# Kernel tuning notes

Hardware: AMD Instinct MI355X
Metric: run time of the kernel (lower is better)

Reference implementation:

```python
import jax, jax.numpy as jnp
import numpy as np

B, TQ, TK, DK, DV = 64, 1024, 1024, 64, 64


def setup_inputs() -> dict:
    key = jax.random.key(0)
    kq, kk, kv, km = jax.random.split(key, 4)
    q = jax.random.normal(kq, (B, TQ, DK), dtype=jnp.float32)
    k = jax.random.normal(kk, (B, TK, DK), dtype=jnp.float32)
    v = jax.random.normal(kv, (B, TK, DV), dtype=jnp.float32)
    mask = jax.random.randint(km, (B, TQ, TK), 0, 2).astype(jnp.int32)
    return {"q": q, "k": k, "v": v, "mask": mask}


def reference(q, k, v, mask):
    # attn = q @ k^T / sqrt(d_k)   -> [B, TQ, TK]
    temper = jnp.sqrt(jnp.asarray(q.shape[-1], dtype=jnp.float32))
    attn = jnp.einsum('bqd,bkd->bqk', q, k) / temper
    # mask-add: -1e9 where mask == 0
    mmask = -1e9 * (1.0 - mask.astype(jnp.float32))
    attn = attn + mmask
    attn = jax.nn.softmax(attn, axis=-1)
    # dropout rate is 0.0 -> identity
    out = jnp.einsum('bqk,bkd->bqd', attn, v)
    return (out, attn)
```

## Files before the change

### kernel.cpp

```cpp
#include <hip/hip_runtime.h>
#include <hip/hip_bf16.h>


#define B_   64
#define TQ_  1024
#define TK_  1024
#define DD   64

typedef short short8 __attribute__((ext_vector_type(8)));
typedef float f32x4 __attribute__((ext_vector_type(4)));

#define PSTR 264
#define WVS  (16 * PSTR)

#define QB_OFF  (0u)
#define KB_OFF  (8u << 20)
#define VT_OFF  (16u << 20)
#define MB_OFF  (24u << 20)
#define WS_NEED (32u << 20)

__device__ __forceinline__ unsigned cvt2(float a, float b) {
    __hip_bfloat162 h = __float22bfloat162_rn(make_float2(a, b));
    unsigned u; __builtin_memcpy(&u, &h, 4); return u;
}
__device__ __forceinline__ short cvt1(float a) {
    __hip_bfloat16 h = __float2bfloat16(a);
    short s; __builtin_memcpy(&s, &h, 2); return s;
}

union Frag { short8 s; unsigned u[4]; };

__global__ __launch_bounds__(256) void prep_kernel(
    const float* __restrict__ qg, const float* __restrict__ kg,
    const float* __restrict__ vg, const int* __restrict__ maskg,
    unsigned char* __restrict__ ws)
{
    const int t = threadIdx.x;
    const int gid = blockIdx.x;
    if (gid < 8192) {
        const int widx = gid * 256 + t;
        const int4* mp = (const int4*)(maskg + (size_t)widx * 32);
        unsigned bits = 0;
        #pragma unroll
        for (int i = 0; i < 8; ++i) {
            const int4 x = mp[i];
            bits |= (unsigned)(x.x & 1) << (4 * i)
                 |  (unsigned)(x.y & 1) << (4 * i + 1)
                 |  (unsigned)(x.z & 1) << (4 * i + 2)
                 |  (unsigned)(x.w & 1) << (4 * i + 3);
        }
        ((unsigned*)(ws + MB_OFF))[widx] = bits;
    } else if (gid < 8192 + 2048) {
        const int i8 = (gid - 8192) * 256 + t;
        const float* p = qg + (size_t)i8 * 8;
        const float4 x = *(const float4*)p, y = *(const float4*)(p + 4);
        uint4 o;
        o.x = cvt2(0.125f * x.x, 0.125f * x.y); o.y = cvt2(0.125f * x.z, 0.125f * x.w);
        o.z = cvt2(0.125f * y.x, 0.125f * y.y); o.w = cvt2(0.125f * y.z, 0.125f * y.w);
        ((uint4*)(ws + QB_OFF))[i8] = o;
    } else if (gid < 8192 + 4096) {
        const int i8 = (gid - 8192 - 2048) * 256 + t;
        const float* p = kg + (size_t)i8 * 8;
        const float4 x = *(const float4*)p, y = *(const float4*)(p + 4);
        uint4 o;
        o.x = cvt2(x.x, x.y); o.y = cvt2(x.z, x.w);
        o.z = cvt2(y.x, y.y); o.w = cvt2(y.z, y.w);
        ((uint4*)(ws + KB_OFF))[i8] = o;
    } else {
        __shared__ short tl[64][72];
        const int b = gid - (8192 + 4096);
        const float* vb = vg + (size_t)b * TK_ * DD;
        short* ob = (short*)(ws + VT_OFF) + (size_t)b * DD * TK_;
        for (int tile = 0; tile < 16; ++tile) {
            const int k0 = tile * 64;
            #pragma unroll
            for (int i = 0; i < 4; ++i) {
                const int row = i * 16 + (t >> 4);
                const int d   = (t & 15) * 4;
                const float4 x = *(const float4*)(vb + (size_t)(k0 + row) * DD + d);
                tl[d + 0][row] = cvt1(x.x); tl[d + 1][row] = cvt1(x.y);
                tl[d + 2][row] = cvt1(x.z); tl[d + 3][row] = cvt1(x.w);
            }
            __syncthreads();
            #pragma unroll
            for (int p = 0; p < 2; ++p) {
                const int d = p * 32 + (t >> 3);
                const uint4 val = *(const uint4*)&tl[d][(t & 7) * 8];
                *(uint4*)(ob + (size_t)d * TK_ + k0 + (t & 7) * 8) = val;
            }
            __syncthreads();
        }
    }
}

__global__ __launch_bounds__(256, 4) void attn_bf16_kernel(
    const unsigned char* __restrict__ ws,
    float* __restrict__ outg, float* __restrict__ attng)
{
    __shared__ __align__(16) short lds[4 * WVS];
    __shared__ float red[128];

    const int t    = threadIdx.x;
    const int wave = t >> 6, lane = t & 63;
    const int quad = lane >> 4, n16 = lane & 15;
    const int b    = blockIdx.y;
    const int q0   = blockIdx.x * 16;
    const int kbase = wave * 256;

    const short*    Qb = (const short*)(ws + QB_OFF);
    const short*    Kb = (const short*)(ws + KB_OFF);
    const short*    Vt = (const short*)(ws + VT_OFF);
    const unsigned* Mb = (const unsigned*)(ws + MB_OFF);

    short* pw = lds + wave * WVS;

    const unsigned* mrow = Mb + ((size_t)(b * TQ_ + q0 + n16)) * 32 + wave * 8;
    const uint4 mw0 = *(const uint4*)(mrow);
    const uint4 mw1 = *(const uint4*)(mrow + 4);

    const short* qp = Qb + ((size_t)(b * TQ_ + q0 + n16)) * DD + quad * 8;
    Frag qf0, qf1;
    qf0.s = *(const short8*)(qp);
    qf1.s = *(const short8*)(qp + 32);

    const short* vrow = Vt + (size_t)b * DD * TK_ + (size_t)n16 * TK_ + kbase + quad * 8;
    Frag vf[4];
    #pragma unroll
    for (int dg = 0; dg < 4; ++dg)
        vf[dg].s = *(const short8*)(vrow + (size_t)(dg * 16) * TK_);

    const short* kbp = Kb + (size_t)(b * TK_ + kbase) * DD;
    Frag kf[16][2];
    #pragma unroll
    for (int kt = 0; kt < 16; ++kt) {
        const short* kp = kbp + (size_t)(kt * 16 + n16) * DD + quad * 8;
        kf[kt][0].s = *(const short8*)(kp);
        kf[kt][1].s = *(const short8*)(kp + 32);
    }

    float s_reg[64];
    const unsigned mwa[8] = {mw0.x, mw0.y, mw0.z, mw0.w, mw1.x, mw1.y, mw1.z, mw1.w};
    #pragma unroll
    for (int kt = 0; kt < 16; ++kt) {
        f32x4 acc = {0.f, 0.f, 0.f, 0.f};
        acc = __builtin_amdgcn_mfma_f32_16x16x32_bf16(kf[kt][0].s, qf0.s, acc, 0, 0, 0);
        acc = __builtin_amdgcn_mfma_f32_16x16x32_bf16(kf[kt][1].s, qf1.s, acc, 0, 0, 0);
        const unsigned m4 = (mwa[kt >> 1] >> (((kt & 1) << 4) | (quad << 2))) & 15u;
        s_reg[kt * 4 + 0] = acc[0] + ((m4 & 1u) ? 0.f : -1e9f);
        s_reg[kt * 4 + 1] = acc[1] + ((m4 & 2u) ? 0.f : -1e9f);
        s_reg[kt * 4 + 2] = acc[2] + ((m4 & 4u) ? 0.f : -1e9f);
        s_reg[kt * 4 + 3] = acc[3] + ((m4 & 8u) ? 0.f : -1e9f);
    }

    float m8[8];
    #pragma unroll
    for (int j = 0; j < 8; ++j) m8[j] = s_reg[j];
    #pragma unroll
    for (int i = 8; i < 64; i += 8)
        #pragma unroll
        for (int j = 0; j < 8; ++j) m8[j] = fmaxf(m8[j], s_reg[i + j]);
    float m = fmaxf(fmaxf(fmaxf(m8[0], m8[1]), fmaxf(m8[2], m8[3])),
                    fmaxf(fmaxf(m8[4], m8[5]), fmaxf(m8[6], m8[7])));
    m = fmaxf(m, __shfl_xor(m, 16));
    m = fmaxf(m, __shfl_xor(m, 32));
    if (lane < 16) red[wave * 16 + n16] = m;
    __syncthreads();
    const float gm = fmaxf(fmaxf(red[n16], red[16 + n16]),
                           fmaxf(red[32 + n16], red[48 + n16]));
    float l0 = 0.f, l1 = 0.f, l2 = 0.f, l3 = 0.f;
    #pragma unroll
    for (int i = 0; i < 16; ++i) {
        const float p0 = __expf(s_reg[4*i+0] - gm);
        const float p1 = __expf(s_reg[4*i+1] - gm);
        const float p2 = __expf(s_reg[4*i+2] - gm);
        const float p3 = __expf(s_reg[4*i+3] - gm);
        s_reg[4*i+0] = p0; s_reg[4*i+1] = p1;
        s_reg[4*i+2] = p2; s_reg[4*i+3] = p3;
        l0 += p0; l1 += p1; l2 += p2; l3 += p3;
    }
    float lsum = (l0 + l1) + (l2 + l3);
    lsum += __shfl_xor(lsum, 16);
    lsum += __shfl_xor(lsum, 32);
    if (lane < 16) red[64 + wave * 16 + n16] = lsum;
    __syncthreads();
    const float inv = 1.f / (red[64 + n16] + red[80 + n16] +
                             red[96 + n16] + red[112 + n16]);
    #pragma unroll
    for (int i = 0; i < 64; ++i) s_reg[i] *= inv;

    float* ab = attng + ((size_t)(b * TQ_ + q0 + n16)) * TK_ + kbase + quad * 4;
    #pragma unroll
    for (int kt = 0; kt < 16; ++kt)
        *(float4*)(ab + kt * 16) = make_float4(s_reg[kt*4+0], s_reg[kt*4+1],
                                               s_reg[kt*4+2], s_reg[kt*4+3]);
    #pragma unroll
    for (int kt = 0; kt < 16; ++kt) {
        uint2 u;
        u.x = cvt2(s_reg[kt*4+0], s_reg[kt*4+1]);
        u.y = cvt2(s_reg[kt*4+2], s_reg[kt*4+3]);
        *(uint2*)(pw + n16 * PSTR + kt * 16 + quad * 4) = u;
    }

    f32x4 oacc[4];
    #pragma unroll
    for (int dg = 0; dg < 4; ++dg) oacc[dg] = (f32x4){0.f, 0.f, 0.f, 0.f};

    #pragma unroll
    for (int c = 0; c < 8; ++c) {
        Frag cur[4];
        #pragma unroll
        for (int dg = 0; dg < 4; ++dg) cur[dg] = vf[dg];
        if (c < 7) {
            #pragma unroll
            for (int dg = 0; dg < 4; ++dg)
                vf[dg].s = *(const short8*)(vrow + (size_t)(dg * 16) * TK_ + (c + 1) * 32);
        }
        Frag pf;
        pf.s = *(const short8*)(pw + n16 * PSTR + c * 32 + quad * 8);
        #pragma unroll
        for (int dg = 0; dg < 4; ++dg)
            oacc[dg] = __builtin_amdgcn_mfma_f32_16x16x32_bf16(cur[dg].s, pf.s, oacc[dg], 0, 0, 0);
    }

    float* ow = (float*)pw;
    #pragma unroll
    for (int dg = 0; dg < 4; ++dg)
        *(f32x4*)&ow[n16 * 68 + dg * 16 + quad * 4] = oacc[dg];
    __syncthreads();
    {
        const int row = t >> 4, col = (t & 15) * 4;
        const float* base = (const float*)lds;
        float4 o = make_float4(0.f, 0.f, 0.f, 0.f);
        #pragma unroll
        for (int w = 0; w < 4; ++w) {
            const float4 x = *(const float4*)(base + w * (WVS / 2) + row * 68 + col);
            o.x += x.x; o.y += x.y; o.z += x.z; o.w += x.w;
        }
        *(float4*)(outg + ((size_t)(b * TQ_ + q0 + row)) * DD + col) = o;
    }
}

__global__ __launch_bounds__(256, 3) void attn_fallback_kernel(
    const float* __restrict__ qg, const float* __restrict__ kg,
    const float* __restrict__ vg, const int* __restrict__ maskg,
    float* __restrict__ outg, float* __restrict__ attng)
{
    __shared__ __align__(16) short lds[4 * WVS];
    __shared__ float red[128];

    const int t    = threadIdx.x;
    const int wave = t >> 6, lane = t & 63;
    const int quad = lane >> 4, n16 = lane & 15;
    const int b    = blockIdx.y;
    const int q0   = blockIdx.x * 16;
    const int kbase = wave * 256;

    short* pw = lds + wave * WVS;

    Frag aq[2];
    {
        const float* qp = qg + ((size_t)(b * TQ_ + q0 + n16)) * DD + quad * 8;
        #pragma unroll
        for (int f = 0; f < 2; ++f) {
            float4 x = *(const float4*)(qp + f * 32);
            float4 y = *(const float4*)(qp + f * 32 + 4);
            aq[f].u[0] = cvt2(0.125f * x.x, 0.125f * x.y);
            aq[f].u[1] = cvt2(0.125f * x.z, 0.125f * x.w);
            aq[f].u[2] = cvt2(0.125f * y.x, 0.125f * y.y);
            aq[f].u[3] = cvt2(0.125f * y.z, 0.125f * y.w);
        }
    }

    float s_reg[64];
    const float* kbp  = kg + (size_t)b * TK_ * DD;
    const int*   mrow = maskg + ((size_t)(b * TQ_ + q0 + n16)) * TK_ + kbase + quad * 4;
    #pragma unroll
    for (int h = 0; h < 2; ++h) {
        int4 mk[8];
        #pragma unroll
        for (int i = 0; i < 8; ++i)
            mk[i] = *(const int4*)(mrow + (h * 8 + i) * 16);
        #pragma unroll
        for (int i = 0; i < 8; ++i) {
            const int kt = h * 8 + i;
            const float* kp = kbp + (size_t)(kbase + kt * 16 + n16) * DD + quad * 8;
            Frag bk[2];
            #pragma unroll
            for (int f = 0; f < 2; ++f) {
                float4 x = *(const float4*)(kp + f * 32);
                float4 y = *(const float4*)(kp + f * 32 + 4);
                bk[f].u[0] = cvt2(x.x, x.y); bk[f].u[1] = cvt2(x.z, x.w);
                bk[f].u[2] = cvt2(y.x, y.y); bk[f].u[3] = cvt2(y.z, y.w);
            }
            f32x4 acc = {0.f, 0.f, 0.f, 0.f};
            acc = __builtin_amdgcn_mfma_f32_16x16x32_bf16(bk[0].s, aq[0].s, acc, 0, 0, 0);
            acc = __builtin_amdgcn_mfma_f32_16x16x32_bf16(bk[1].s, aq[1].s, acc, 0, 0, 0);
            s_reg[kt * 4 + 0] = acc[0] + (mk[i].x ? 0.f : -1e9f);
            s_reg[kt * 4 + 1] = acc[1] + (mk[i].y ? 0.f : -1e9f);
            s_reg[kt * 4 + 2] = acc[2] + (mk[i].z ? 0.f : -1e9f);
            s_reg[kt * 4 + 3] = acc[3] + (mk[i].w ? 0.f : -1e9f);
        }
    }

    const float* vb0 = vg + (size_t)b * TK_ * DD + (size_t)(kbase + quad * 8) * DD + n16;
    float vraw[32];
    #pragma unroll
    for (int u = 0; u < 32; ++u)
        vraw[u] = vb0[(size_t)(u & 7) * DD + (u >> 3) * 16];

    float m8[8];
    #pragma unroll
    for (int j = 0; j < 8; ++j) m8[j] = s_reg[j];
    #pragma unroll
    for (int i = 8; i < 64; i += 8)
        #pragma unroll
        for (int j = 0; j < 8; ++j) m8[j] = fmaxf(m8[j], s_reg[i + j]);
    float m = fmaxf(fmaxf(fmaxf(m8[0], m8[1]), fmaxf(m8[2], m8[3])),
                    fmaxf(fmaxf(m8[4], m8[5]), fmaxf(m8[6], m8[7])));
    m = fmaxf(m, __shfl_xor(m, 16));
    m = fmaxf(m, __shfl_xor(m, 32));
    if (lane < 16) red[wave * 16 + n16] = m;
    __syncthreads();
    const float gm = fmaxf(fmaxf(red[n16], red[16 + n16]),
                           fmaxf(red[32 + n16], red[48 + n16]));
    float l0 = 0.f, l1 = 0.f, l2 = 0.f, l3 = 0.f;
    #pragma unroll
    for (int i = 0; i < 16; ++i) {
        const float p0 = __expf(s_reg[4*i+0] - gm);
        const float p1 = __expf(s_reg[4*i+1] - gm);
        const float p2 = __expf(s_reg[4*i+2] - gm);
        const float p3 = __expf(s_reg[4*i+3] - gm);
        s_reg[4*i+0] = p0; s_reg[4*i+1] = p1;
        s_reg[4*i+2] = p2; s_reg[4*i+3] = p3;
        l0 += p0; l1 += p1; l2 += p2; l3 += p3;
    }
    float lsum = (l0 + l1) + (l2 + l3);
    lsum += __shfl_xor(lsum, 16);
    lsum += __shfl_xor(lsum, 32);
    if (lane < 16) red[64 + wave * 16 + n16] = lsum;
    __syncthreads();
    const float inv = 1.f / (red[64 + n16] + red[80 + n16] +
                             red[96 + n16] + red[112 + n16]);
    #pragma unroll
    for (int i = 0; i < 64; ++i) s_reg[i] *= inv;

    float* ab = attng + ((size_t)(b * TQ_ + q0 + n16)) * TK_ + kbase + quad * 4;
    #pragma unroll
    for (int kt = 0; kt < 16; ++kt)
        *(float4*)(ab + kt * 16) = make_float4(s_reg[kt*4+0], s_reg[kt*4+1],
                                               s_reg[kt*4+2], s_reg[kt*4+3]);
    #pragma unroll
    for (int kt = 0; kt < 16; ++kt) {
        uint2 u;
        u.x = cvt2(s_reg[kt*4+0], s_reg[kt*4+1]);
        u.y = cvt2(s_reg[kt*4+2], s_reg[kt*4+3]);
        *(uint2*)(pw + n16 * PSTR + kt * 16 + quad * 4) = u;
    }

    f32x4 oacc[4];
    #pragma unroll
    for (int dg = 0; dg < 4; ++dg) oacc[dg] = (f32x4){0.f, 0.f, 0.f, 0.f};

    #pragma unroll
    for (int c = 0; c < 8; ++c) {
        unsigned va16[16];
        #pragma unroll
        for (int dg = 0; dg < 4; ++dg)
            #pragma unroll
            for (int w = 0; w < 4; ++w)
                va16[dg * 4 + w] = cvt2(vraw[dg * 8 + 2 * w], vraw[dg * 8 + 2 * w + 1]);
        if (c < 7) {
            #pragma unroll
            for (int u = 0; u < 32; ++u)
                vraw[u] = vb0[(size_t)((c + 1) * 32 + (u & 7)) * DD + (u >> 3) * 16];
        }
        Frag pf;
        pf.s = *(const short8*)(pw + n16 * PSTR + c * 32 + quad * 8);
        #pragma unroll
        for (int dg = 0; dg < 4; ++dg) {
            Frag af;
            af.u[0] = va16[dg*4+0]; af.u[1] = va16[dg*4+1];
            af.u[2] = va16[dg*4+2]; af.u[3] = va16[dg*4+3];
            oacc[dg] = __builtin_amdgcn_mfma_f32_16x16x32_bf16(af.s, pf.s, oacc[dg], 0, 0, 0);
        }
    }

    float* ow = (float*)pw;
    #pragma unroll
    for (int dg = 0; dg < 4; ++dg)
        *(f32x4*)&ow[n16 * 68 + dg * 16 + quad * 4] = oacc[dg];
    __syncthreads();
    {
        const int row = t >> 4, col = (t & 15) * 4;
        const float* base = (const float*)lds;
        float4 o = make_float4(0.f, 0.f, 0.f, 0.f);
        #pragma unroll
        for (int w = 0; w < 4; ++w) {
            const float4 x = *(const float4*)(base + w * (WVS / 2) + row * 68 + col);
            o.x += x.x; o.y += x.y; o.z += x.z; o.w += x.w;
        }
        *(float4*)(outg + ((size_t)(b * TQ_ + q0 + row)) * DD + col) = o;
    }
}

extern "C" void kernel_launch(void* const* d_in, const int* in_sizes, int n_in,
                              void* d_out, int out_size, void* d_ws, size_t ws_size,
                              hipStream_t stream) {
    const float* q    = (const float*)d_in[0];
    const float* k    = (const float*)d_in[1];
    const float* v    = (const float*)d_in[2];
    const int*   mask = (const int*)d_in[3];

    float* out  = (float*)d_out;
    float* attn = out + (size_t)B_ * TQ_ * DD;

    if (ws_size >= (size_t)WS_NEED && d_ws != nullptr) {
        unsigned char* ws = (unsigned char*)d_ws;
        prep_kernel<<<dim3(12352), 256, 0, stream>>>(q, k, v, mask, ws);
        attn_bf16_kernel<<<dim3(TQ_ / 16, B_), 256, 0, stream>>>(ws, out, attn);
    } else {
        attn_fallback_kernel<<<dim3(TQ_ / 16, B_), 256, 0, stream>>>(q, k, v, mask, out, attn);
    }
}
```

Measured before the change: 634.6 us.

## Halve per-wave P staging LDS and split V transpose across more blocks

The bf16 attention kernel now stages the probability tile in two halves of 128 keys each. It reuses a 68-word-stride buffer, which roughly halves LDS per block and is meant to allow more resident blocks per CU. The PV MFMA loop becomes two 4-step passes with a re-fill of the LDS buffer between them. The prep kernel's V transpose is spread over 1024 blocks of one 64-key tile each, instead of 64 blocks looping over 16 tiles, which removes a serial tail in the prep kernel.

```diff
diff --git a/kernel.cpp b/kernel.cpp
--- a/kernel.cpp
+++ b/kernel.cpp
@@ -10,8 +10,8 @@
 typedef short short8 __attribute__((ext_vector_type(8)));
 typedef float f32x4 __attribute__((ext_vector_type(4)));
 
-#define PSTR 264
-#define WVS  (16 * PSTR)
+#define PLW    68
+#define PL_U32 (16 * PLW)
 
 #define QB_OFF  (0u)
 #define KB_OFF  (8u << 20)
@@ -37,8 +37,29 @@
 {
     const int t = threadIdx.x;
     const int gid = blockIdx.x;
-    if (gid < 8192) {
-        const int widx = gid * 256 + t;
+    if (gid < 1024) {
+        __shared__ short tl[64][72];
+        const int b  = gid >> 4;
+        const int k0 = (gid & 15) * 64;
+        const float* vb = vg + (size_t)b * TK_ * DD;
+        short* ob = (short*)(ws + VT_OFF) + (size_t)b * DD * TK_;
+        #pragma unroll
+        for (int i = 0; i < 4; ++i) {
+            const int row = i * 16 + (t >> 4);
+            const int d   = (t & 15) * 4;
+            const float4 x = *(const float4*)(vb + (size_t)(k0 + row) * DD + d);
+            tl[d + 0][row] = cvt1(x.x); tl[d + 1][row] = cvt1(x.y);
+            tl[d + 2][row] = cvt1(x.z); tl[d + 3][row] = cvt1(x.w);
+        }
+        __syncthreads();
+        #pragma unroll
+        for (int p = 0; p < 2; ++p) {
+            const int d = p * 32 + (t >> 3);
+            const uint4 val = *(const uint4*)&tl[d][(t & 7) * 8];
+            *(uint4*)(ob + (size_t)d * TK_ + k0 + (t & 7) * 8) = val;
+        }
+    } else if (gid < 1024 + 8192) {
+        const int widx = (gid - 1024) * 256 + t;
         const int4* mp = (const int4*)(maskg + (size_t)widx * 32);
         unsigned bits = 0;
         #pragma unroll
@@ -50,46 +71,22 @@
                  |  (unsigned)(x.w & 1) << (4 * i + 3);
         }
         ((unsigned*)(ws + MB_OFF))[widx] = bits;
-    } else if (gid < 8192 + 2048) {
-        const int i8 = (gid - 8192) * 256 + t;
+    } else if (gid < 1024 + 8192 + 2048) {
+        const int i8 = (gid - 1024 - 8192) * 256 + t;
         const float* p = qg + (size_t)i8 * 8;
         const float4 x = *(const float4*)p, y = *(const float4*)(p + 4);
         uint4 o;
         o.x = cvt2(0.125f * x.x, 0.125f * x.y); o.y = cvt2(0.125f * x.z, 0.125f * x.w);
         o.z = cvt2(0.125f * y.x, 0.125f * y.y); o.w = cvt2(0.125f * y.z, 0.125f * y.w);
         ((uint4*)(ws + QB_OFF))[i8] = o;
-    } else if (gid < 8192 + 4096) {
-        const int i8 = (gid - 8192 - 2048) * 256 + t;
+    } else {
+        const int i8 = (gid - 1024 - 8192 - 2048) * 256 + t;
         const float* p = kg + (size_t)i8 * 8;
         const float4 x = *(const float4*)p, y = *(const float4*)(p + 4);
         uint4 o;
         o.x = cvt2(x.x, x.y); o.y = cvt2(x.z, x.w);
         o.z = cvt2(y.x, y.y); o.w = cvt2(y.z, y.w);
         ((uint4*)(ws + KB_OFF))[i8] = o;
-    } else {
-        __shared__ short tl[64][72];
-        const int b = gid - (8192 + 4096);
-        const float* vb = vg + (size_t)b * TK_ * DD;
-        short* ob = (short*)(ws + VT_OFF) + (size_t)b * DD * TK_;
-        for (int tile = 0; tile < 16; ++tile) {
-            const int k0 = tile * 64;
-            #pragma unroll
-            for (int i = 0; i < 4; ++i) {
-                const int row = i * 16 + (t >> 4);
-                const int d   = (t & 15) * 4;
-                const float4 x = *(const float4*)(vb + (size_t)(k0 + row) * DD + d);
-                tl[d + 0][row] = cvt1(x.x); tl[d + 1][row] = cvt1(x.y);
-                tl[d + 2][row] = cvt1(x.z); tl[d + 3][row] = cvt1(x.w);
-            }
-            __syncthreads();
-            #pragma unroll
-            for (int p = 0; p < 2; ++p) {
-                const int d = p * 32 + (t >> 3);
-                const uint4 val = *(const uint4*)&tl[d][(t & 7) * 8];
-                *(uint4*)(ob + (size_t)d * TK_ + k0 + (t & 7) * 8) = val;
-            }
-            __syncthreads();
-        }
     }
 }
 
@@ -97,7 +94,7 @@
     const unsigned char* __restrict__ ws,
     float* __restrict__ outg, float* __restrict__ attng)
 {
-    __shared__ __align__(16) short lds[4 * WVS];
+    __shared__ __align__(16) unsigned lds[4 * PL_U32];
     __shared__ float red[128];
 
     const int t    = threadIdx.x;
@@ -112,7 +109,7 @@
     const short*    Vt = (const short*)(ws + VT_OFF);
     const unsigned* Mb = (const unsigned*)(ws + MB_OFF);
 
-    short* pw = lds + wave * WVS;
+    unsigned* pl = lds + wave * PL_U32;
 
     const unsigned* mrow = Mb + ((size_t)(b * TQ_ + q0 + n16)) * 32 + wave * 8;
     const uint4 mw0 = *(const uint4*)(mrow);
@@ -194,11 +191,11 @@
         *(float4*)(ab + kt * 16) = make_float4(s_reg[kt*4+0], s_reg[kt*4+1],
                                                s_reg[kt*4+2], s_reg[kt*4+3]);
     #pragma unroll
-    for (int kt = 0; kt < 16; ++kt) {
+    for (int kt = 0; kt < 8; ++kt) {
         uint2 u;
         u.x = cvt2(s_reg[kt*4+0], s_reg[kt*4+1]);
         u.y = cvt2(s_reg[kt*4+2], s_reg[kt*4+3]);
-        *(uint2*)(pw + n16 * PSTR + kt * 16 + quad * 4) = u;
+        *(uint2*)&pl[n16 * PLW + kt * 8 + quad * 2] = u;
     }
 
     f32x4 oacc[4];
@@ -206,26 +203,49 @@
     for (int dg = 0; dg < 4; ++dg) oacc[dg] = (f32x4){0.f, 0.f, 0.f, 0.f};
 
     #pragma unroll
-    for (int c = 0; c < 8; ++c) {
+    for (int c = 0; c < 4; ++c) {
         Frag cur[4];
         #pragma unroll
         for (int dg = 0; dg < 4; ++dg) cur[dg] = vf[dg];
-        if (c < 7) {
+        #pragma unroll
+        for (int dg = 0; dg < 4; ++dg)
+            vf[dg].s = *(const short8*)(vrow + (size_t)(dg * 16) * TK_ + (c + 1) * 32);
+        Frag pf;
+        pf.s = *(const short8*)&pl[n16 * PLW + c * 16 + quad * 4];
+        #pragma unroll
+        for (int dg = 0; dg < 4; ++dg)
+            oacc[dg] = __builtin_amdgcn_mfma_f32_16x16x32_bf16(cur[dg].s, pf.s, oacc[dg], 0, 0, 0);
+    }
+
+    #pragma unroll
+    for (int kt = 8; kt < 16; ++kt) {
+        uint2 u;
+        u.x = cvt2(s_reg[kt*4+0], s_reg[kt*4+1]);
+        u.y = cvt2(s_reg[kt*4+2], s_reg[kt*4+3]);
+        *(uint2*)&pl[n16 * PLW + (kt - 8) * 8 + quad * 2] = u;
+    }
+
+    #pragma unroll
+    for (int c = 0; c < 4; ++c) {
+        Frag cur[4];
+        #pragma unroll
+        for (int dg = 0; dg < 4; ++dg) cur[dg] = vf[dg];
+        if (c < 3) {
             #pragma unroll
             for (int dg = 0; dg < 4; ++dg)
-                vf[dg].s = *(const short8*)(vrow + (size_t)(dg * 16) * TK_ + (c + 1) * 32);
+                vf[dg].s = *(const short8*)(vrow + (size_t)(dg * 16) * TK_ + (c + 5) * 32);
         }
         Frag pf;
-        pf.s = *(const short8*)(pw + n16 * PSTR + c * 32 + quad * 8);
+        pf.s = *(const short8*)&pl[n16 * PLW + c * 16 + quad * 4];
         #pragma unroll
         for (int dg = 0; dg < 4; ++dg)
             oacc[dg] = __builtin_amdgcn_mfma_f32_16x16x32_bf16(cur[dg].s, pf.s, oacc[dg], 0, 0, 0);
     }
 
-    float* ow = (float*)pw;
+    float* ow = (float*)pl;
     #pragma unroll
     for (int dg = 0; dg < 4; ++dg)
-        *(f32x4*)&ow[n16 * 68 + dg * 16 + quad * 4] = oacc[dg];
+        *(f32x4*)&ow[n16 * PLW + dg * 16 + quad * 4] = oacc[dg];
     __syncthreads();
     {
         const int row = t >> 4, col = (t & 15) * 4;
@@ -233,19 +253,22 @@
         float4 o = make_float4(0.f, 0.f, 0.f, 0.f);
         #pragma unroll
         for (int w = 0; w < 4; ++w) {
-            const float4 x = *(const float4*)(base + w * (WVS / 2) + row * 68 + col);
+            const float4 x = *(const float4*)(base + w * PL_U32 + row * PLW + col);
             o.x += x.x; o.y += x.y; o.z += x.z; o.w += x.w;
         }
         *(float4*)(outg + ((size_t)(b * TQ_ + q0 + row)) * DD + col) = o;
     }
 }
+
+#define PSTR 264
+#define FWVS (16 * PSTR)
 
 __global__ __launch_bounds__(256, 3) void attn_fallback_kernel(
     const float* __restrict__ qg, const float* __restrict__ kg,
     const float* __restrict__ vg, const int* __restrict__ maskg,
     float* __restrict__ outg, float* __restrict__ attng)
 {
-    __shared__ __align__(16) short lds[4 * WVS];
+    __shared__ __align__(16) short lds[4 * FWVS];
     __shared__ float red[128];
 
     const int t    = threadIdx.x;
@@ -255,7 +278,7 @@
     const int q0   = blockIdx.x * 16;
     const int kbase = wave * 256;
 
-    short* pw = lds + wave * WVS;
+    short* pw = lds + wave * FWVS;
 
     Frag aq[2];
     {
@@ -396,7 +419,7 @@
         float4 o = make_float4(0.f, 0.f, 0.f, 0.f);
         #pragma unroll
         for (int w = 0; w < 4; ++w) {
-            const float4 x = *(const float4*)(base + w * (WVS / 2) + row * 68 + col);
+            const float4 x = *(const float4*)(base + w * (FWVS / 2) + row * 68 + col);
             o.x += x.x; o.y += x.y; o.z += x.z; o.w += x.w;
         }
         *(float4*)(outg + ((size_t)(b * TQ_ + q0 + row)) * DD + col) = o;
@@ -416,7 +439,7 @@
 
     if (ws_size >= (size_t)WS_NEED && d_ws != nullptr) {
         unsigned char* ws = (unsigned char*)d_ws;
-        prep_kernel<<<dim3(12352), 256, 0, stream>>>(q, k, v, mask, ws);
+        prep_kernel<<<dim3(13312), 256, 0, stream>>>(q, k, v, mask, ws);
         attn_bf16_kernel<<<dim3(TQ_ / 16, B_), 256, 0, stream>>>(ws, out, attn);
     } else {
         attn_fallback_kernel<<<dim3(TQ_ / 16, B_), 256, 0, stream>>>(q, k, v, mask, out, attn);
```

Result: faster. 615.7 us (-3.0%).
